# Kernel optimization log

Measured on AMD Instinct MI355X. Metric: run time of the kernel, lower is better.

Reference implementation:

```python
import jax, jax.numpy as jnp
import numpy as np

N = 262144
D = 128  # hidden_dim
NUM_RULES = 5


def setup_inputs() -> dict:
    key = jax.random.key(0)
    ks = jax.random.split(key, 7)
    h_fused = jax.random.normal(ks[0], (N, D), dtype=jnp.float32)
    entity_types = jax.random.randint(ks[1], (N,), 0, 3)
    entity_masks = jnp.ones((N,), dtype=bool)
    # rule_scorer params (torch nn.Linear convention: y = x @ W.T + b)
    W1 = jax.random.normal(ks[2], (D, 3 * D), dtype=jnp.float32) * (1.0 / np.sqrt(3 * D))
    b1 = jnp.zeros((D,), dtype=jnp.float32)
    W2 = jax.random.normal(ks[3], (1, D), dtype=jnp.float32) * (1.0 / np.sqrt(D))
    b2 = jnp.zeros((1,), dtype=jnp.float32)
    rule_table = jax.random.normal(ks[4], (NUM_RULES, D), dtype=jnp.float32) * 0.1
    return {"h_fused": h_fused, "entity_types": entity_types,
            "entity_masks": entity_masks, "rule_id": 0,
            "W1": W1, "b1": b1, "W2": W2, "b2": b2, "rule_table": rule_table}


def reference(h_fused, entity_types, entity_masks, rule_id, W1, b1, W2, b2, rule_table):
    # masks per entity type
    car_mask = (entity_types == 0) & entity_masks
    light_mask = (entity_types == 1) & entity_masks
    stop_mask = (entity_types == 2) & entity_masks

    def masked_mean(mask):
        mf = mask.astype(h_fused.dtype)[:, None]            # [N,1]
        cnt = mf.sum()
        s = (h_fused * mf).sum(axis=0)                      # [D]
        return jnp.where(cnt > 0, s / jnp.maximum(cnt, 1.0), 0.0)

    h_light = masked_mean(light_mask)  # [D] - pooled once (original redundantly recomputes per car)
    h_stop = masked_mean(stop_mask)    # [D]

    n = h_fused.shape[0]
    concat = jnp.concatenate([
        h_fused,
        jnp.broadcast_to(h_light, (n, D)),
        jnp.broadcast_to(h_stop, (n, D)),
    ], axis=1)                                              # [N, 3D]

    hid = jax.nn.relu(concat @ W1.T + b1)                   # [N, D] (dropout = identity, eval)
    beta = jax.nn.sigmoid(hid @ W2.T + b2)[:, 0]            # [N]

    rule_emb = rule_table[rule_id]                          # [D]
    h_car = beta[:, None] * h_fused + (1.0 - beta[:, None]) * rule_emb
    h_out = jnp.where(car_mask[:, None], h_car, h_fused)    # [N, D]
    beta_out = jnp.where(car_mask, beta, 0.0)               # [N]; original compacts to [N_car]
    return h_out, beta_out
```

## Files before the change

kernel.cpp:

```cpp
#include <hip/hip_runtime.h>
#include <hip/hip_bf16.h>

#define D 128

typedef __attribute__((ext_vector_type(8))) short short8;
typedef __attribute__((ext_vector_type(4))) float f32x4;

__device__ __forceinline__ unsigned short f2bf(float f) {
  unsigned int u = __float_as_uint(f);
  u += 0x7FFFu + ((u >> 16) & 1u);
  return (unsigned short)(u >> 16);
}

__device__ __forceinline__ bool mask_at(const unsigned char* m, int i, bool i32layout) {
  return i32layout ? (((const int*)m)[i] != 0) : (m[i] != 0);
}


__global__ __launch_bounds__(256) void k_reduce(
    const float* __restrict__ h, const int* __restrict__ types,
    const unsigned char* __restrict__ masks, float* __restrict__ ws) {
  const int t = threadIdx.x;
  const int c4 = t & 31;
  const int rgrp = t >> 5;
  const int row0 = blockIdx.x * 256;
  const bool mi32 = (masks[1] == 0);
  __shared__ float wl_s[256], ws_s[256];
  __shared__ float redL[8][128], redS[8][128];
  {
    const int r = row0 + t;
    const int ty = types[r];
    const bool m = mask_at(masks, r, mi32);
    wl_s[t] = (ty == 1 && m) ? 1.f : 0.f;
    ws_s[t] = (ty == 2 && m) ? 1.f : 0.f;
  }
  __syncthreads();
  f32x4 sl = {0.f, 0.f, 0.f, 0.f}, ss = {0.f, 0.f, 0.f, 0.f};
  #pragma unroll 4
  for (int i = 0; i < 32; ++i) {
    const int rl = rgrp + 8 * i;
    const f32x4 v = *(const f32x4*)&h[(size_t)(row0 + rl) * D + c4 * 4];
    const float wl = wl_s[rl];
    const float w2 = ws_s[rl];
    sl += v * wl;
    ss += v * w2;
  }
  *(f32x4*)&redL[rgrp][c4 * 4] = sl;
  *(f32x4*)&redS[rgrp][c4 * 4] = ss;
  __syncthreads();
  {
    const int arr = t >> 7, col = t & 127;
    float s = 0.f;
    #pragma unroll
    for (int g = 0; g < 8; ++g) s += arr ? redS[g][col] : redL[g][col];
    atomicAdd(&ws[arr * 128 + col], s);
  }
  if (t < 64) {
    float c = wl_s[t] + wl_s[t + 64] + wl_s[t + 128] + wl_s[t + 192];
    #pragma unroll
    for (int m = 1; m < 64; m <<= 1) c += __shfl_xor(c, m, 64);
    if (t == 0) atomicAdd(&ws[256], c);
  } else if (t < 128) {
    const int u = t - 64;
    float c = ws_s[u] + ws_s[u + 64] + ws_s[u + 128] + ws_s[u + 192];
    #pragma unroll
    for (int m = 1; m < 64; m <<= 1) c += __shfl_xor(c, m, 64);
    if (t == 64) atomicAdd(&ws[257], c);
  }
}

__global__ __launch_bounds__(256, 2) void k_main(
    const float* __restrict__ h, const int* __restrict__ types,
    const unsigned char* __restrict__ masks,
    const int* __restrict__ rid_p,
    const float* __restrict__ W1, const float* __restrict__ b1,
    const float* __restrict__ W2, const float* __restrict__ b2p,
    const float* __restrict__ rule_table,
    const float* __restrict__ ws,
    float* __restrict__ out_h, float* __restrict__ out_beta) {
  __shared__ __align__(16) unsigned short Bs[128][136];
  __shared__ __align__(16) unsigned short As[2][64][136];
  __shared__ float cs_s[128], w2_s[128], rule_s[128];
  __shared__ float betas[2][64], car_s[2][64];
  __shared__ float hl_s[128], hs_s[128], partial[256];

  const int t = threadIdx.x;
  const int wave = t >> 6;
  const int lane = t & 63;
  const int lrow = lane & 15;
  const int q = lane >> 4;
  const bool mi32 = (masks[1] == 0);
  const int base = blockIdx.x * 256;

  #pragma unroll
  for (int i = 0; i < 16; ++i) {
    const int idx = (i * 256 + t) * 4;
    const int j = idx >> 7, k = idx & 127;
    const f32x4 w = *(const f32x4*)&W1[j * 384 + k];
    ushort4 bv;
    bv.x = f2bf(w.x); bv.y = f2bf(w.y); bv.z = f2bf(w.z); bv.w = f2bf(w.w);
    *(ushort4*)&Bs[j][k] = bv;
  }

  {
    const float cl = ws[256], cst = ws[257];
    if (t < 128) {
      hl_s[t] = (cl > 0.f) ? ws[t] / cl : 0.f;
    } else {
      const int u = t - 128;
      hs_s[u] = (cst > 0.f) ? ws[128 + u] / cst : 0.f;
    }
    __syncthreads();
    const int j = t & 127, half = t >> 7;
    const float* wrow = W1 + j * 384 + 128 + half * 128;
    const float* hv = half ? hs_s : hl_s;
    float acc = 0.f;
    #pragma unroll 8
    for (int kk = 0; kk < 32; ++kk) {
      const f32x4 w = *(const f32x4*)&wrow[kk * 4];
      acc += w.x * hv[kk * 4 + 0] + w.y * hv[kk * 4 + 1] +
             w.z * hv[kk * 4 + 2] + w.w * hv[kk * 4 + 3];
    }
    partial[t] = acc;
    __syncthreads();
    if (t < 128) {
      cs_s[t] = partial[t] + partial[t + 128] + b1[t];
      w2_s[t] = W2[t];
      rule_s[t] = rule_table[rid_p[0] * D + t];
    }
  }

  const float b2v = b2p[0];

  f32x4 st[8];
  #pragma unroll
  for (int i = 0; i < 8; ++i) {
    const int flat = i * 256 + t;
    const int r = flat >> 5, cc4 = flat & 31;
    st[i] = *(const f32x4*)&h[(size_t)(base + r) * D + cc4 * 4];
  }
  #pragma unroll
  for (int i = 0; i < 8; ++i) {
    const int flat = i * 256 + t;
    const int r = flat >> 5, cc4 = flat & 31;
    ushort4 bv;
    bv.x = f2bf(st[i].x); bv.y = f2bf(st[i].y);
    bv.z = f2bf(st[i].z); bv.w = f2bf(st[i].w);
    *(ushort4*)&As[0][r][cc4 * 4] = bv;
  }
  __syncthreads();

  for (int tile = 0; tile < 4; ++tile) {
    const int p = tile & 1;
    const int row0 = base + tile * 64;

    if (tile < 3) {
      const int row0n = row0 + 64;
      #pragma unroll
      for (int i = 0; i < 8; ++i) {
        const int flat = i * 256 + t;
        const int r = flat >> 5, cc4 = flat & 31;
        st[i] = *(const f32x4*)&h[(size_t)(row0n + r) * D + cc4 * 4];
      }
    }

    if (t < 64) {
      const int grow = row0 + t;
      car_s[p][t] = ((types[grow] == 0) && mask_at(masks, grow, mi32)) ? 1.f : 0.f;
    }

    short8 a[4];
    #pragma unroll
    for (int ks = 0; ks < 4; ++ks)
      a[ks] = *(const short8*)&As[p][wave * 16 + lrow][ks * 32 + q * 8];

    f32x4 acc[8];
    #pragma unroll
    for (int nt = 0; nt < 8; ++nt) acc[nt] = (f32x4){0.f, 0.f, 0.f, 0.f};
    #pragma unroll
    for (int nt = 0; nt < 8; ++nt) {
      #pragma unroll
      for (int ks = 0; ks < 4; ++ks)
        acc[nt] = __builtin_amdgcn_mfma_f32_16x16x32_bf16(
            a[ks], *(const short8*)&Bs[nt * 16 + lrow][ks * 32 + q * 8],
            acc[nt], 0, 0, 0);
    }

    float part[4] = {0.f, 0.f, 0.f, 0.f};
    #pragma unroll
    for (int nt = 0; nt < 8; ++nt) {
      const int col = nt * 16 + lrow;
      const float cv = cs_s[col];
      const float wv = w2_s[col];
      #pragma unroll
      for (int r = 0; r < 4; ++r)
        part[r] += fmaxf(acc[nt][r] + cv, 0.f) * wv;
    }
    #pragma unroll
    for (int m = 1; m < 16; m <<= 1) {
      #pragma unroll
      for (int r = 0; r < 4; ++r) part[r] += __shfl_xor(part[r], m, 64);
    }
    if (lrow == 0) {
      #pragma unroll
      for (int r = 0; r < 4; ++r) {
        const float z = part[r] + b2v;
        betas[p][wave * 16 + q * 4 + r] = 1.f / (1.f + __expf(-z));
      }
    }
    __syncthreads();

    #pragma unroll
    for (int i = 0; i < 4; ++i) {
      const int flat8 = i * 256 + t;
      const int r = flat8 >> 4, c8 = flat8 & 15;
      const uint4 u = *(const uint4*)&As[p][r][c8 * 8];
      const float beta = betas[p][r];
      const float cf = car_s[p][r];
      const float a_r = cf * beta + (1.f - cf);
      const float b_r = cf * (1.f - beta);
      f32x4 o0, o1;
      o0.x = a_r * __uint_as_float(u.x << 16)          + b_r * rule_s[c8 * 8 + 0];
      o0.y = a_r * __uint_as_float(u.x & 0xFFFF0000u)  + b_r * rule_s[c8 * 8 + 1];
      o0.z = a_r * __uint_as_float(u.y << 16)          + b_r * rule_s[c8 * 8 + 2];
      o0.w = a_r * __uint_as_float(u.y & 0xFFFF0000u)  + b_r * rule_s[c8 * 8 + 3];
      o1.x = a_r * __uint_as_float(u.z << 16)          + b_r * rule_s[c8 * 8 + 4];
      o1.y = a_r * __uint_as_float(u.z & 0xFFFF0000u)  + b_r * rule_s[c8 * 8 + 5];
      o1.z = a_r * __uint_as_float(u.w << 16)          + b_r * rule_s[c8 * 8 + 6];
      o1.w = a_r * __uint_as_float(u.w & 0xFFFF0000u)  + b_r * rule_s[c8 * 8 + 7];
      float* op = &out_h[(size_t)(row0 + r) * D + c8 * 8];
      __builtin_nontemporal_store(o0, (f32x4*)op);
      __builtin_nontemporal_store(o1, (f32x4*)(op + 4));
    }
    if (t < 64)
      __builtin_nontemporal_store(car_s[p][t] * betas[p][t], &out_beta[row0 + t]);

    if (tile < 3) {
      #pragma unroll
      for (int i = 0; i < 8; ++i) {
        const int flat = i * 256 + t;
        const int r = flat >> 5, cc4 = flat & 31;
        ushort4 bv;
        bv.x = f2bf(st[i].x); bv.y = f2bf(st[i].y);
        bv.z = f2bf(st[i].z); bv.w = f2bf(st[i].w);
        *(ushort4*)&As[p ^ 1][r][cc4 * 4] = bv;
      }
      __syncthreads();
    }
  }
}

extern "C" void kernel_launch(void* const* d_in, const int* in_sizes, int n_in,
                              void* d_out, int out_size, void* d_ws, size_t ws_size,
                              hipStream_t stream) {
  const float* h = (const float*)d_in[0];
  const int* types = (const int*)d_in[1];
  const unsigned char* masks = (const unsigned char*)d_in[2];
  const int* rid = (const int*)d_in[3];
  const float* W1 = (const float*)d_in[4];
  const float* b1 = (const float*)d_in[5];
  const float* W2 = (const float*)d_in[6];
  const float* b2 = (const float*)d_in[7];
  const float* rule_table = (const float*)d_in[8];
  float* ws = (float*)d_ws;
  const int n = in_sizes[0] / D;
  float* out_h = (float*)d_out;
  float* out_beta = out_h + (size_t)n * D;

  hipMemsetAsync(d_ws, 0, 258 * sizeof(float), stream);
  k_reduce<<<n / 256, 256, 0, stream>>>(h, types, masks, ws);
  k_main<<<n / 256, 256, 0, stream>>>(h, types, masks, rid, W1, b1, W2, b2,
                                      rule_table, ws, out_h, out_beta);
}
```

Baseline: 307.8 us.

## Single-buffer the activation tile and overlay scratch to fit three blocks per CU

Drops the double-buffered As tile down to one buffer and places the pooled-mean and partial-sum scratch arrays inside As, cutting LDS use so launch bounds can ask for three blocks per CU. So the single buffer can be refilled safely, each tile's epilogue values are read from As into registers before the MFMA loop, and the barrier now runs every iteration. The first h tile load is also issued at kernel start so it overlaps the W1 conversion. The intent is more resident waves to hide memory latency, at the cost of extra registers and a barrier per tile, and 1024 blocks may leave a tail on the last dispatch round.

```diff
diff --git a/kernel.cpp b/kernel.cpp
--- a/kernel.cpp
+++ b/kernel.cpp
@@ -69,7 +69,7 @@
   }
 }
 
-__global__ __launch_bounds__(256, 2) void k_main(
+__global__ __launch_bounds__(256, 3) void k_main(
     const float* __restrict__ h, const int* __restrict__ types,
     const unsigned char* __restrict__ masks,
     const int* __restrict__ rid_p,
@@ -79,10 +79,9 @@
     const float* __restrict__ ws,
     float* __restrict__ out_h, float* __restrict__ out_beta) {
   __shared__ __align__(16) unsigned short Bs[128][136];
-  __shared__ __align__(16) unsigned short As[2][64][136];
+  __shared__ __align__(16) unsigned short As[64][136];
   __shared__ float cs_s[128], w2_s[128], rule_s[128];
-  __shared__ float betas[2][64], car_s[2][64];
-  __shared__ float hl_s[128], hs_s[128], partial[256];
+  __shared__ float betas[64], car_s[64];
 
   const int t = threadIdx.x;
   const int wave = t >> 6;
@@ -91,6 +90,19 @@
   const int q = lane >> 4;
   const bool mi32 = (masks[1] == 0);
   const int base = blockIdx.x * 256;
+
+  float* ovl = (float*)&As[0][0];
+  float* hl_s = ovl;
+  float* hs_s = ovl + 128;
+  float* partial = ovl + 256;
+
+  f32x4 st[8];
+  #pragma unroll
+  for (int i = 0; i < 8; ++i) {
+    const int flat = i * 256 + t;
+    const int r = flat >> 5, cc4 = flat & 31;
+    st[i] = *(const f32x4*)&h[(size_t)(base + r) * D + cc4 * 4];
+  }
 
   #pragma unroll
   for (int i = 0; i < 16; ++i) {
@@ -128,17 +140,11 @@
       w2_s[t] = W2[t];
       rule_s[t] = rule_table[rid_p[0] * D + t];
     }
+    __syncthreads();
   }
 
   const float b2v = b2p[0];
 
-  f32x4 st[8];
-  #pragma unroll
-  for (int i = 0; i < 8; ++i) {
-    const int flat = i * 256 + t;
-    const int r = flat >> 5, cc4 = flat & 31;
-    st[i] = *(const f32x4*)&h[(size_t)(base + r) * D + cc4 * 4];
-  }
   #pragma unroll
   for (int i = 0; i < 8; ++i) {
     const int flat = i * 256 + t;
@@ -146,12 +152,11 @@
     ushort4 bv;
     bv.x = f2bf(st[i].x); bv.y = f2bf(st[i].y);
     bv.z = f2bf(st[i].z); bv.w = f2bf(st[i].w);
-    *(ushort4*)&As[0][r][cc4 * 4] = bv;
+    *(ushort4*)&As[r][cc4 * 4] = bv;
   }
   __syncthreads();
 
   for (int tile = 0; tile < 4; ++tile) {
-    const int p = tile & 1;
     const int row0 = base + tile * 64;
 
     if (tile < 3) {
@@ -166,13 +171,21 @@
 
     if (t < 64) {
       const int grow = row0 + t;
-      car_s[p][t] = ((types[grow] == 0) && mask_at(masks, grow, mi32)) ? 1.f : 0.f;
+      car_s[t] = ((types[grow] == 0) && mask_at(masks, grow, mi32)) ? 1.f : 0.f;
     }
 
     short8 a[4];
     #pragma unroll
     for (int ks = 0; ks < 4; ++ks)
-      a[ks] = *(const short8*)&As[p][wave * 16 + lrow][ks * 32 + q * 8];
+      a[ks] = *(const short8*)&As[wave * 16 + lrow][ks * 32 + q * 8];
+
+    uint4 u[4];
+    #pragma unroll
+    for (int i = 0; i < 4; ++i) {
+      const int flat8 = i * 256 + t;
+      const int r = flat8 >> 4, c8 = flat8 & 15;
+      u[i] = *(const uint4*)&As[r][c8 * 8];
+    }
 
     f32x4 acc[8];
     #pragma unroll
@@ -205,7 +218,7 @@
       #pragma unroll
       for (int r = 0; r < 4; ++r) {
         const float z = part[r] + b2v;
-        betas[p][wave * 16 + q * 4 + r] = 1.f / (1.f + __expf(-z));
+        betas[wave * 16 + q * 4 + r] = 1.f / (1.f + __expf(-z));
       }
     }
     __syncthreads();
@@ -214,26 +227,25 @@
     for (int i = 0; i < 4; ++i) {
       const int flat8 = i * 256 + t;
       const int r = flat8 >> 4, c8 = flat8 & 15;
-      const uint4 u = *(const uint4*)&As[p][r][c8 * 8];
-      const float beta = betas[p][r];
-      const float cf = car_s[p][r];
+      const float beta = betas[r];
+      const float cf = car_s[r];
       const float a_r = cf * beta + (1.f - cf);
       const float b_r = cf * (1.f - beta);
       f32x4 o0, o1;
-      o0.x = a_r * __uint_as_float(u.x << 16)          + b_r * rule_s[c8 * 8 + 0];
-      o0.y = a_r * __uint_as_float(u.x & 0xFFFF0000u)  + b_r * rule_s[c8 * 8 + 1];
-      o0.z = a_r * __uint_as_float(u.y << 16)          + b_r * rule_s[c8 * 8 + 2];
-      o0.w = a_r * __uint_as_float(u.y & 0xFFFF0000u)  + b_r * rule_s[c8 * 8 + 3];
-      o1.x = a_r * __uint_as_float(u.z << 16)          + b_r * rule_s[c8 * 8 + 4];
-      o1.y = a_r * __uint_as_float(u.z & 0xFFFF0000u)  + b_r * rule_s[c8 * 8 + 5];
-      o1.z = a_r * __uint_as_float(u.w << 16)          + b_r * rule_s[c8 * 8 + 6];
-      o1.w = a_r * __uint_as_float(u.w & 0xFFFF0000u)  + b_r * rule_s[c8 * 8 + 7];
+      o0.x = a_r * __uint_as_float(u[i].x << 16)          + b_r * rule_s[c8 * 8 + 0];
+      o0.y = a_r * __uint_as_float(u[i].x & 0xFFFF0000u)  + b_r * rule_s[c8 * 8 + 1];
+      o0.z = a_r * __uint_as_float(u[i].y << 16)          + b_r * rule_s[c8 * 8 + 2];
+      o0.w = a_r * __uint_as_float(u[i].y & 0xFFFF0000u)  + b_r * rule_s[c8 * 8 + 3];
+      o1.x = a_r * __uint_as_float(u[i].z << 16)          + b_r * rule_s[c8 * 8 + 4];
+      o1.y = a_r * __uint_as_float(u[i].z & 0xFFFF0000u)  + b_r * rule_s[c8 * 8 + 5];
+      o1.z = a_r * __uint_as_float(u[i].w << 16)          + b_r * rule_s[c8 * 8 + 6];
+      o1.w = a_r * __uint_as_float(u[i].w & 0xFFFF0000u)  + b_r * rule_s[c8 * 8 + 7];
       float* op = &out_h[(size_t)(row0 + r) * D + c8 * 8];
       __builtin_nontemporal_store(o0, (f32x4*)op);
       __builtin_nontemporal_store(o1, (f32x4*)(op + 4));
     }
     if (t < 64)
-      __builtin_nontemporal_store(car_s[p][t] * betas[p][t], &out_beta[row0 + t]);
+      __builtin_nontemporal_store(car_s[t] * betas[t], &out_beta[row0 + t]);
 
     if (tile < 3) {
       #pragma unroll
@@ -243,10 +255,10 @@
         ushort4 bv;
         bv.x = f2bf(st[i].x); bv.y = f2bf(st[i].y);
         bv.z = f2bf(st[i].z); bv.w = f2bf(st[i].w);
-        *(ushort4*)&As[p ^ 1][r][cc4 * 4] = bv;
+        *(ushort4*)&As[r][cc4 * 4] = bv;
       }
-      __syncthreads();
-    }
+    }
+    __syncthreads();
   }
 }
 
```

New measurement: 308.9 us. Within noise of the previous version (+0.4%).
